# Kernel optimization log

Hardware: AMD Instinct MI355X
Metric: run time of the kernel (lower is better)

The kernel has to match this reference:

```python
import jax, jax.numpy as jnp
import numpy as np

B, S, H = 2, 512, 768
E, M, R, R2 = 64, 64, 128, 128
NER_C, REL_C, SIZE_E, CLS = 10, 8, 32, 101
NEG = -1e30


def _linear(x, w, b):
    # torch nn.Linear convention: w is [out, in]
    return x @ w.T + b


def _span_pool(emb, masks):
    # emb [B,S,H], masks [B,K,S] -> masked max over tokens -> [B,K,H]
    neg = jnp.where(masks[..., None] != 0, 0.0, NEG)  # [B,K,S,1]
    return jnp.max(neg + emb[:, None, :, :], axis=2)


def _classify_spans(input_ids, emb, masks, size_emb, rep_w, rep_b, head_w, head_b):
    pool = _span_pool(emb, masks)                      # [B,K,H]
    cls_idx = jnp.argmax((input_ids == CLS).astype(jnp.int32), axis=1)
    ctx = emb[jnp.arange(emb.shape[0]), cls_idx]       # [B,H] (get_token)
    rep = jnp.concatenate([jnp.broadcast_to(ctx[:, None, :], pool.shape), pool, size_emb], axis=-1)
    clf = _linear(jax.nn.relu(_linear(rep, rep_w, rep_b)), head_w, head_b)
    return clf, pool


def _classify_relations(pool, size_emb, rels, rel_masks, emb, w1, b1, w2, b2, w3, b3):
    Bc = pool.shape[0]
    bidx = jnp.arange(Bc)[:, None, None]
    pairs = pool[bidx, rels].reshape(Bc, rels.shape[1], -1)        # [B,R,2H]
    size_pairs = size_emb[bidx, rels].reshape(Bc, rels.shape[1], -1)  # [B,R,2*SIZE_E]
    # masked max over context tokens (rel mask)
    ctx = jnp.max(jnp.where(rel_masks[..., None] != 0, 0.0, NEG) + emb[:, None, :, :], axis=2)
    ctx = jnp.where(jnp.any(rel_masks != 0, axis=-1)[..., None], ctx, 0.0)
    rel_repr = jnp.concatenate([ctx, pairs, size_pairs], axis=-1)  # [B,R,3H+2*SIZE_E]
    h = jax.nn.relu(_linear(rel_repr, w1, b1))
    h = jax.nn.relu(_linear(h, w2, b2))
    return _linear(h, w3, b3)


def setup_inputs():
    key = jax.random.key(0)
    ks = jax.random.split(key, 24)
    p = lambda k, shape: jax.random.normal(k, shape, jnp.float32) * 0.02
    ids = jax.random.randint(ks[0], (B, S), 2000, 30000)
    ids = ids.at[:, 0].set(CLS)  # exactly one cls token per row
    return dict(
        input_ids=ids,
        entity_masks=jax.random.randint(ks[1], (B, E, S), 0, 2).astype(jnp.int32),
        entity_sizes=jax.random.randint(ks[2], (B, E), 0, 100),
        mention_masks=jax.random.randint(ks[3], (B, M, S), 0, 2).astype(jnp.int32),
        mention_sizes=jax.random.randint(ks[4], (B, M), 0, 100),
        relations=jax.random.randint(ks[5], (B, R, 2), 0, E),
        rel_masks=jax.random.randint(ks[6], (B, R, S), 0, 2).astype(jnp.int32),
        references=jax.random.randint(ks[7], (B, R2, 2), 0, M),
        references_masks=jax.random.randint(ks[8], (B, R2, S), 0, 2).astype(jnp.int32),
        token_embedding=jax.random.normal(ks[9], (B, S, H), jnp.float32),
        ner_size_emb=p(ks[10], (100, SIZE_E)),
        emd_size_emb=p(ks[11], (100, SIZE_E)),
        ner_rep_w=p(ks[12], (H, 2 * H + SIZE_E)), ner_rep_b=jnp.zeros(H, jnp.float32),
        ner_head_w=p(ks[13], (NER_C, H)), ner_head_b=jnp.zeros(NER_C, jnp.float32),
        emd_rep_w=p(ks[14], (H, 2 * H + SIZE_E)), emd_rep_b=jnp.zeros(H, jnp.float32),
        emd_head_w=p(ks[15], (2, H)), emd_head_b=jnp.zeros(2, jnp.float32),
        rel_w1=p(ks[16], (H, 3 * H + 2 * SIZE_E)), rel_b1=jnp.zeros(H, jnp.float32),
        rel_w2=p(ks[17], (H, H)), rel_b2=jnp.zeros(H, jnp.float32),
        rel_w3=p(ks[18], (REL_C, H)), rel_b3=jnp.zeros(REL_C, jnp.float32),
        cr_w1=p(ks[19], (H, 3 * H + 2 * SIZE_E)), cr_b1=jnp.zeros(H, jnp.float32),
        cr_w2=p(ks[20], (H, H)), cr_b2=jnp.zeros(H, jnp.float32),
        cr_w3=p(ks[21], (1, H)), cr_b3=jnp.zeros(1, jnp.float32),
    )


def reference(input_ids, entity_masks, entity_sizes, mention_masks, mention_sizes,
              relations, rel_masks, references, references_masks, token_embedding,
              ner_size_emb, emd_size_emb,
              ner_rep_w, ner_rep_b, ner_head_w, ner_head_b,
              emd_rep_w, emd_rep_b, emd_head_w, emd_head_b,
              rel_w1, rel_b1, rel_w2, rel_b2, rel_w3, rel_b3,
              cr_w1, cr_b1, cr_w2, cr_b2, cr_w3, cr_b3):
    sz = ner_size_emb[entity_sizes]                                    # [B,E,SIZE_E]
    entity_clf, entity_pool = _classify_spans(input_ids, token_embedding, entity_masks, sz,
                                              ner_rep_w, ner_rep_b, ner_head_w, ner_head_b)
    rel_clf = _classify_relations(entity_pool, sz, relations, rel_masks, token_embedding,
                                  rel_w1, rel_b1, rel_w2, rel_b2, rel_w3, rel_b3)
    msz = emd_size_emb[mention_sizes]
    mention_clf, mention_pool = _classify_spans(input_ids, token_embedding, mention_masks, msz,
                                                emd_rep_w, emd_rep_b, emd_head_w, emd_head_b)
    ref_clf = _classify_relations(mention_pool, msz, references, references_masks, token_embedding,
                                  cr_w1, cr_b1, cr_w2, cr_b2, cr_w3, cr_b3)
    return entity_clf, rel_clf, mention_clf, ref_clf
```

## Files before the change

kernel.cpp:

```cpp
#include <hip/hip_runtime.h>
#include <hip/hip_bf16.h>

typedef __hip_bfloat16 bf16;
typedef __attribute__((ext_vector_type(8))) short short8;
typedef __attribute__((ext_vector_type(4))) float f32x4;

#define SS 512
#define HD 768
#define NEGC (-1e30f)

#define WOFF_NER 0
#define WOFF_EMD 1204224
#define WOFF_RW1 2408448
#define WOFF_CW1 4227072
#define WOFF_RW2 6045696
#define WOFF_CW2 6635520
#define W_TOT    7225344
#define CVT_BLOCKS (W_TOT / 4 / 256)

__global__ __launch_bounds__(256) void k_pool_cvt(
    const int* __restrict__ e_masks, const int* __restrict__ m_masks,
    const int* __restrict__ r_masks, const int* __restrict__ c_masks,
    const float* __restrict__ emb, bf16* __restrict__ part, int* __restrict__ flags,
    const float* __restrict__ s0, const float* __restrict__ s1,
    const float* __restrict__ s2, const float* __restrict__ s3,
    const float* __restrict__ s4, const float* __restrict__ s5,
    bf16* __restrict__ wdst)
{
  int bx = blockIdx.x;
  int t  = threadIdx.x;

  if (bx >= 768) {
    size_t i = ((size_t)(bx - 768) * 256 + t) * 4;
    const float* s; size_t off;
    if      (i < WOFF_EMD) { s = s0; off = i; }
    else if (i < WOFF_RW1) { s = s1; off = i - WOFF_EMD; }
    else if (i < WOFF_CW1) { s = s2; off = i - WOFF_RW1; }
    else if (i < WOFF_RW2) { s = s3; off = i - WOFF_CW1; }
    else if (i < WOFF_CW2) { s = s4; off = i - WOFF_RW2; }
    else                   { s = s5; off = i - WOFF_CW2; }
    float4 v = *(const float4*)(s + off);
    wdst[i]     = __hip_bfloat16(v.x);
    wdst[i + 1] = __hip_bfloat16(v.y);
    wdst[i + 2] = __hip_bfloat16(v.z);
    wdst[i + 3] = __hip_bfloat16(v.w);
    return;
  }

  int g  = bx % 48;
  int b  = (bx / 48) & 1;
  int sp = bx / 96;
  int j0 = g * 8;

  const int* marr; int row0;
  if      (j0 < 64)  { marr = e_masks; row0 = b*64  +  j0;        }
  else if (j0 < 128) { marr = m_masks; row0 = b*64  + (j0-64);    }
  else if (j0 < 256) { marr = r_masks; row0 = b*128 + (j0-128);   }
  else               { marr = c_masks; row0 = b*128 + (j0-256);   }

  __shared__ unsigned s_pack[64];
  __shared__ unsigned s_any;
  if (t == 0) s_any = 0u;
  __syncthreads();

  int sbase = sp * 64;
  if (t < 64) {
    unsigned w = 0;
    #pragma unroll
    for (int k = 0; k < 8; k++) {
      int mm = marr[(size_t)(row0 + k) * SS + sbase + t];
      w |= (mm != 0 ? 1u : 0u) << k;
    }
    s_pack[t] = w;
    atomicOr(&s_any, w);
  }
  __syncthreads();

  float acc[8][3];
  #pragma unroll
  for (int k = 0; k < 8; k++)
    #pragma unroll
    for (int i = 0; i < 3; i++) acc[k][i] = -INFINITY;

  const float* ebase = emb + ((size_t)b * SS + sbase) * HD;
  for (int s = 0; s < 64; s++) {
    unsigned wm = s_pack[s];
    const float* ep = ebase + (size_t)s * HD + t;
    float v0 = ep[0];
    float v1 = ep[256];
    float v2 = ep[512];
    #pragma unroll
    for (int k = 0; k < 8; k++) {
      float add = ((wm >> k) & 1u) ? 0.f : NEGC;
      acc[k][0] = fmaxf(acc[k][0], v0 + add);
      acc[k][1] = fmaxf(acc[k][1], v1 + add);
      acc[k][2] = fmaxf(acc[k][2], v2 + add);
    }
  }

  #pragma unroll
  for (int k = 0; k < 8; k++) {
    int sg = b * 384 + j0 + k;
    bf16* dst = part + ((size_t)sp * 768 + sg) * HD;
    dst[t]       = __hip_bfloat16(acc[k][0]);
    dst[t + 256] = __hip_bfloat16(acc[k][1]);
    dst[t + 512] = __hip_bfloat16(acc[k][2]);
  }
  if (t < 8) flags[sp * 768 + b * 384 + j0 + t] = (int)((s_any >> t) & 1u);
}

__global__ __launch_bounds__(256) void k_combine(
    const bf16* __restrict__ part, const int* __restrict__ flags,
    bf16* __restrict__ epool, bf16* __restrict__ mpool,
    bf16* __restrict__ rctx, bf16* __restrict__ cctx)
{
  int sg = blockIdx.x;
  int b = sg / 384, j = sg % 384;
  int any = 0;
  #pragma unroll
  for (int sp = 0; sp < 8; sp++) any |= flags[sp * 768 + sg];
  #pragma unroll
  for (int i = 0; i < 3; i++) {
    int h = threadIdx.x + i * 256;
    float v = -INFINITY;
    #pragma unroll
    for (int sp = 0; sp < 8; sp++)
      v = fmaxf(v, (float)part[((size_t)sp * 768 + sg) * HD + h]);
    if      (j < 64)  epool[((size_t)b*64  + j)       * HD + h] = __hip_bfloat16(v);
    else if (j < 128) mpool[((size_t)b*64  + (j-64))  * HD + h] = __hip_bfloat16(v);
    else if (j < 256) rctx [((size_t)b*128 + (j-128)) * HD + h] = __hip_bfloat16(any ? v : 0.f);
    else              cctx [((size_t)b*128 + (j-256)) * HD + h] = __hip_bfloat16(any ? v : 0.f);
  }
}

__global__ __launch_bounds__(256) void k_rep(
    const int* __restrict__ input_ids, const float* __restrict__ emb,
    const bf16* __restrict__ epool, const bf16* __restrict__ mpool,
    const bf16* __restrict__ rctx, const bf16* __restrict__ cctx,
    const int* __restrict__ esizes, const int* __restrict__ msizes,
    const float* __restrict__ nsemb, const float* __restrict__ esemb,
    const int* __restrict__ relations, const int* __restrict__ references,
    bf16* __restrict__ nrep, bf16* __restrict__ erep,
    bf16* __restrict__ rrep, bf16* __restrict__ crep)
{
  int mode = blockIdx.y;
  if (mode < 2) {
    if (blockIdx.x >= 128) return;
    int which = mode;
    int row = blockIdx.x;
    int b = row >> 6;
    const bf16*  pool  = which ? mpool  : epool;
    const int*   sizes = which ? msizes : esizes;
    const float* st    = which ? esemb  : nsemb;
    bf16* rep = (which ? erep : nrep) + (size_t)row * 1568;

    __shared__ int s_cls;
    if (threadIdx.x == 0) s_cls = SS;
    __syncthreads();
    for (int s = threadIdx.x; s < SS; s += 256)
      if (input_ids[b * SS + s] == 101) atomicMin(&s_cls, s);
    __syncthreads();
    int ci = (s_cls == SS) ? 0 : s_cls;

    const float* ctx = emb + ((size_t)b * SS + ci) * HD;
    const bf16*  pl  = pool + (size_t)row * HD;
    for (int h = threadIdx.x; h < HD; h += 256) {
      rep[h]       = __hip_bfloat16(ctx[h]);
      rep[768 + h] = pl[h];
    }
    if (threadIdx.x < 32)
      rep[1536 + threadIdx.x] = __hip_bfloat16(st[(size_t)sizes[row] * 32 + threadIdx.x]);
  } else {
    int which = mode - 2;
    int row = blockIdx.x;
    int b = row >> 7;
    const int*   rel   = which ? references : relations;
    const bf16*  ctx   = which ? cctx   : rctx;
    const bf16*  pool  = which ? mpool  : epool;
    const int*   sizes = which ? msizes : esizes;
    const float* st    = which ? esemb  : nsemb;
    bf16* rep = (which ? crep : rrep) + (size_t)row * 2368;

    int a0 = rel[row * 2], a1 = rel[row * 2 + 1];
    const bf16* p0 = pool + ((size_t)b * 64 + a0) * HD;
    const bf16* p1 = pool + ((size_t)b * 64 + a1) * HD;
    const bf16* cx = ctx + (size_t)row * HD;
    for (int h = threadIdx.x; h < HD; h += 256) {
      rep[h]        = cx[h];
      rep[768 + h]  = p0[h];
      rep[1536 + h] = p1[h];
    }
    if (threadIdx.x < 32) {
      rep[2304 + threadIdx.x] = __hip_bfloat16(st[(size_t)sizes[b * 64 + a0] * 32 + threadIdx.x]);
      rep[2336 + threadIdx.x] = __hip_bfloat16(st[(size_t)sizes[b * 64 + a1] * 32 + threadIdx.x]);
    }
  }
}

struct GemmArgs  { const void* A; const void* W; const float* bias; void* C; int K; int M; int store_bf16; };
struct GemmArgs4 { GemmArgs p[4]; };

__global__ __launch_bounds__(256) void k_gemm4(GemmArgs4 ga)
{
  GemmArgs g = ga.p[blockIdx.z];
  int mt = blockIdx.x * 32;
  if (mt >= g.M) return;
  int nt = blockIdx.y * 32;

  const short* A = (const short*)g.A;
  const short* W = (const short*)g.W;
  int K_ = g.K;

  int wave = threadIdx.x >> 6, lane = threadIdx.x & 63;
  int lm = lane & 15, quad = lane >> 4;

  const short* a0p = A + (size_t)(mt + lm)      * K_ + quad * 8;
  const short* a1p = A + (size_t)(mt + 16 + lm) * K_ + quad * 8;
  const short* w0p = W + (size_t)(nt + lm)      * K_ + quad * 8;
  const short* w1p = W + (size_t)(nt + 16 + lm) * K_ + quad * 8;

  f32x4 acc00 = {0.f,0.f,0.f,0.f}, acc01 = {0.f,0.f,0.f,0.f};
  f32x4 acc10 = {0.f,0.f,0.f,0.f}, acc11 = {0.f,0.f,0.f,0.f};

  for (int k0 = wave * 32; k0 < K_; k0 += 128) {
    short8 a0 = *(const short8*)(a0p + k0);
    short8 a1 = *(const short8*)(a1p + k0);
    short8 w0 = *(const short8*)(w0p + k0);
    short8 w1 = *(const short8*)(w1p + k0);
    acc00 = __builtin_amdgcn_mfma_f32_16x16x32_bf16(a0, w0, acc00, 0, 0, 0);
    acc01 = __builtin_amdgcn_mfma_f32_16x16x32_bf16(a0, w1, acc01, 0, 0, 0);
    acc10 = __builtin_amdgcn_mfma_f32_16x16x32_bf16(a1, w0, acc10, 0, 0, 0);
    acc11 = __builtin_amdgcn_mfma_f32_16x16x32_bf16(a1, w1, acc11, 0, 0, 0);
  }

  __shared__ float red[4][32][32];
  #pragma unroll
  for (int reg = 0; reg < 4; reg++) {
    int r = quad * 4 + reg;
    red[wave][r][lm]           = acc00[reg];
    red[wave][r][16 + lm]      = acc01[reg];
    red[wave][16 + r][lm]      = acc10[reg];
    red[wave][16 + r][16 + lm] = acc11[reg];
  }
  __syncthreads();

  int c = threadIdx.x & 31;
  int rb = threadIdx.x >> 5;
  float bb = g.bias[nt + c];
  #pragma unroll
  for (int i = 0; i < 4; i++) {
    int r = rb + 8 * i;
    float v = red[0][r][c] + red[1][r][c] + red[2][r][c] + red[3][r][c];
    v = fmaxf(v + bb, 0.f);
    if (g.store_bf16) ((bf16*)g.C)[(size_t)(mt + r) * HD + nt + c] = __hip_bfloat16(v);
    else              ((float*)g.C)[(size_t)(mt + r) * HD + nt + c] = v;
  }
}

__global__ __launch_bounds__(256) void k_heads(
    const float* __restrict__ NH, const float* __restrict__ EH,
    const float* __restrict__ RH2, const float* __restrict__ CH2,
    const float* __restrict__ nhw, const float* __restrict__ nhb,
    const float* __restrict__ ehw, const float* __restrict__ ehb,
    const float* __restrict__ rw3, const float* __restrict__ rb3,
    const float* __restrict__ cw3, const float* __restrict__ cb3,
    float* __restrict__ out)
{
  int gr = blockIdx.x;
  const float* A; const float* W; const float* Bb; float* op; int N;
  if (gr < 128)      { A = NH  + (size_t)gr * HD;        W = nhw; Bb = nhb; N = 10; op = out + (size_t)gr * 10; }
  else if (gr < 384) { int r = gr - 128; A = RH2 + (size_t)r * HD; W = rw3; Bb = rb3; N = 8; op = out + 1280 + (size_t)r * 8; }
  else if (gr < 512) { int r = gr - 384; A = EH  + (size_t)r * HD; W = ehw; Bb = ehb; N = 2; op = out + 3328 + (size_t)r * 2; }
  else               { int r = gr - 512; A = CH2 + (size_t)r * HD; W = cw3; Bb = cb3; N = 1; op = out + 3584 + (size_t)r; }

  float acc[10];
  #pragma unroll
  for (int o = 0; o < 10; o++) acc[o] = 0.f;

  for (int k = threadIdx.x; k < HD; k += 256) {
    float a = A[k];
    #pragma unroll
    for (int o = 0; o < 10; o++) {
      int oo = (o < N) ? o : 0;
      acc[o] += a * W[(size_t)oo * HD + k];
    }
  }

  __shared__ float red[4][10];
  int lane = threadIdx.x & 63, wv = threadIdx.x >> 6;
  #pragma unroll
  for (int o = 0; o < 10; o++) {
    float v = acc[o];
    for (int off = 32; off > 0; off >>= 1) v += __shfl_down(v, off);
    if (lane == 0) red[wv][o] = v;
  }
  __syncthreads();
  if (threadIdx.x < N) {
    float v = red[0][threadIdx.x] + red[1][threadIdx.x] + red[2][threadIdx.x] +
              red[3][threadIdx.x] + Bb[threadIdx.x];
    op[threadIdx.x] = v;
  }
}

extern "C" void kernel_launch(void* const* d_in, const int* in_sizes, int n_in,
                              void* d_out, int out_size, void* d_ws, size_t ws_size,
                              hipStream_t stream)
{
  const int*   input_ids  = (const int*)d_in[0];
  const int*   e_masks    = (const int*)d_in[1];
  const int*   e_sizes    = (const int*)d_in[2];
  const int*   m_masks    = (const int*)d_in[3];
  const int*   m_sizes    = (const int*)d_in[4];
  const int*   relations  = (const int*)d_in[5];
  const int*   r_masks    = (const int*)d_in[6];
  const int*   references = (const int*)d_in[7];
  const int*   c_masks    = (const int*)d_in[8];
  const float* emb        = (const float*)d_in[9];
  const float* nsemb      = (const float*)d_in[10];
  const float* esemb      = (const float*)d_in[11];
  const float* ner_rep_w  = (const float*)d_in[12];
  const float* ner_rep_b  = (const float*)d_in[13];
  const float* ner_head_w = (const float*)d_in[14];
  const float* ner_head_b = (const float*)d_in[15];
  const float* emd_rep_w  = (const float*)d_in[16];
  const float* emd_rep_b  = (const float*)d_in[17];
  const float* emd_head_w = (const float*)d_in[18];
  const float* emd_head_b = (const float*)d_in[19];
  const float* rel_w1 = (const float*)d_in[20];
  const float* rel_b1 = (const float*)d_in[21];
  const float* rel_w2 = (const float*)d_in[22];
  const float* rel_b2 = (const float*)d_in[23];
  const float* rel_w3 = (const float*)d_in[24];
  const float* rel_b3 = (const float*)d_in[25];
  const float* cr_w1 = (const float*)d_in[26];
  const float* cr_b1 = (const float*)d_in[27];
  const float* cr_w2 = (const float*)d_in[28];
  const float* cr_b2 = (const float*)d_in[29];
  const float* cr_w3 = (const float*)d_in[30];
  const float* cr_b3 = (const float*)d_in[31];
  float* out = (float*)d_out;

  float* wsf = (float*)d_ws;
  size_t o = 0;
  int*   FLAGS = (int*)(wsf + o); o += 8 * 768;
  float* NH  = wsf + o; o += (size_t)128 * HD;
  float* EH  = wsf + o; o += (size_t)128 * HD;
  float* RH2 = wsf + o; o += (size_t)256 * HD;
  float* CH2 = wsf + o; o += (size_t)256 * HD;

  bf16* wsb = (bf16*)(wsf + o);
  size_t ob = 0;
  bf16* WBF   = wsb + ob; ob += (size_t)W_TOT;
  bf16* PART  = wsb + ob; ob += (size_t)8 * 768 * HD;
  bf16* EPOOL = wsb + ob; ob += (size_t)128 * HD;
  bf16* MPOOL = wsb + ob; ob += (size_t)128 * HD;
  bf16* RCTX  = wsb + ob; ob += (size_t)256 * HD;
  bf16* CCTX  = wsb + ob; ob += (size_t)256 * HD;
  bf16* NREP  = wsb + ob; ob += (size_t)128 * 1568;
  bf16* EREP  = wsb + ob; ob += (size_t)128 * 1568;
  bf16* RREP  = wsb + ob; ob += (size_t)256 * 2368;
  bf16* CREP  = wsb + ob; ob += (size_t)256 * 2368;
  bf16* RH1   = wsb + ob; ob += (size_t)256 * HD;
  bf16* CH1   = wsb + ob; ob += (size_t)256 * HD;

  k_pool_cvt<<<768 + CVT_BLOCKS, 256, 0, stream>>>(
      e_masks, m_masks, r_masks, c_masks, emb, PART, FLAGS,
      ner_rep_w, emd_rep_w, rel_w1, cr_w1, rel_w2, cr_w2, WBF);
  k_combine<<<768, 256, 0, stream>>>(PART, FLAGS, EPOOL, MPOOL, RCTX, CCTX);
  k_rep<<<dim3(256, 4), 256, 0, stream>>>(input_ids, emb, EPOOL, MPOOL, RCTX, CCTX,
                                          e_sizes, m_sizes, nsemb, esemb,
                                          relations, references,
                                          NREP, EREP, RREP, CREP);
  {
    GemmArgs4 ga;
    ga.p[0] = { NREP, WBF + WOFF_NER, ner_rep_b, NH,  1568, 128, 0 };
    ga.p[1] = { EREP, WBF + WOFF_EMD, emd_rep_b, EH,  1568, 128, 0 };
    ga.p[2] = { RREP, WBF + WOFF_RW1, rel_b1,    RH1, 2368, 256, 1 };
    ga.p[3] = { CREP, WBF + WOFF_CW1, cr_b1,     CH1, 2368, 256, 1 };
    k_gemm4<<<dim3(8, 24, 4), 256, 0, stream>>>(ga);
  }
  {
    GemmArgs4 ga;
    ga.p[0] = { RH1, WBF + WOFF_RW2, rel_b2, RH2, 768, 256, 0 };
    ga.p[1] = { CH1, WBF + WOFF_CW2, cr_b2,  CH2, 768, 256, 0 };
    ga.p[2] = ga.p[0]; ga.p[3] = ga.p[1];
    k_gemm4<<<dim3(8, 24, 2), 256, 0, stream>>>(ga);
  }
  k_heads<<<768, 256, 0, stream>>>(NH, EH, RH2, CH2,
                                   ner_head_w, ner_head_b, emd_head_w, emd_head_b,
                                   rel_w3, rel_b3, cr_w3, cr_b3, out);
}
```

Measured before the change: 209.2 us.

## Fuse post-pool stages into persistent megakernel with grid barriers, split pooling finer

Replaces the combine, rep-building, two GEMM and head kernels with one persistent 768-block kernel that separates stages with a software grid barrier built on global atomics. This removes several kernel launches and their gaps. The pooling kernel now splits tokens into 16 chunks of 32 instead of 8 of 64, and weight conversion is spread across the pool blocks with a strided loop. The barrier depends on all 768 blocks being co-resident (launch bounds ask for 3 blocks per CU), and the finer split doubles the partial-buffer traffic.

```diff
diff --git a/kernel.cpp b/kernel.cpp
--- a/kernel.cpp
+++ b/kernel.cpp
@@ -8,6 +8,9 @@
 #define SS 512
 #define HD 768
 #define NEGC (-1e30f)
+#define NSPLIT 16
+#define TOK 32
+#define POOL_BLOCKS 1536
 
 #define WOFF_NER 0
 #define WOFF_EMD 1204224
@@ -16,7 +19,29 @@
 #define WOFF_RW2 6045696
 #define WOFF_CW2 6635520
 #define W_TOT    7225344
-#define CVT_BLOCKS (W_TOT / 4 / 256)
+#define CVT_UNITS (W_TOT / 1024)
+
+__device__ unsigned d_cnt = 0;
+__device__ unsigned d_gen = 0;
+
+__device__ __forceinline__ void grid_bar(int nblk)
+{
+  __syncthreads();
+  if (threadIdx.x == 0) {
+    __threadfence();
+    unsigned g = atomicAdd(&d_gen, 0u);
+    unsigned t = atomicAdd(&d_cnt, 1u);
+    if (t == (unsigned)(nblk - 1)) {
+      atomicExch(&d_cnt, 0u);
+      __threadfence();
+      atomicAdd(&d_gen, 1u);
+    } else {
+      while (atomicAdd(&d_gen, 0u) == g) { __builtin_amdgcn_s_sleep(2); }
+    }
+    __threadfence();
+  }
+  __syncthreads();
+}
 
 __global__ __launch_bounds__(256) void k_pool_cvt(
     const int* __restrict__ e_masks, const int* __restrict__ m_masks,
@@ -30,8 +55,8 @@
   int bx = blockIdx.x;
   int t  = threadIdx.x;
 
-  if (bx >= 768) {
-    size_t i = ((size_t)(bx - 768) * 256 + t) * 4;
+  for (int u = bx; u < CVT_UNITS; u += POOL_BLOCKS) {
+    size_t i = ((size_t)u * 256 + t) * 4;
     const float* s; size_t off;
     if      (i < WOFF_EMD) { s = s0; off = i; }
     else if (i < WOFF_RW1) { s = s1; off = i - WOFF_EMD; }
@@ -44,7 +69,6 @@
     wdst[i + 1] = __hip_bfloat16(v.y);
     wdst[i + 2] = __hip_bfloat16(v.z);
     wdst[i + 3] = __hip_bfloat16(v.w);
-    return;
   }
 
   int g  = bx % 48;
@@ -58,13 +82,13 @@
   else if (j0 < 256) { marr = r_masks; row0 = b*128 + (j0-128);   }
   else               { marr = c_masks; row0 = b*128 + (j0-256);   }
 
-  __shared__ unsigned s_pack[64];
+  __shared__ unsigned s_pack[TOK];
   __shared__ unsigned s_any;
   if (t == 0) s_any = 0u;
   __syncthreads();
 
-  int sbase = sp * 64;
-  if (t < 64) {
+  int sbase = sp * TOK;
+  if (t < TOK) {
     unsigned w = 0;
     #pragma unroll
     for (int k = 0; k < 8; k++) {
@@ -83,7 +107,7 @@
     for (int i = 0; i < 3; i++) acc[k][i] = -INFINITY;
 
   const float* ebase = emb + ((size_t)b * SS + sbase) * HD;
-  for (int s = 0; s < 64; s++) {
+  for (int s = 0; s < TOK; s++) {
     unsigned wm = s_pack[s];
     const float* ep = ebase + (size_t)s * HD + t;
     float v0 = ep[0];
@@ -109,104 +133,28 @@
   if (t < 8) flags[sp * 768 + b * 384 + j0 + t] = (int)((s_any >> t) & 1u);
 }
 
-__global__ __launch_bounds__(256) void k_combine(
-    const bf16* __restrict__ part, const int* __restrict__ flags,
-    bf16* __restrict__ epool, bf16* __restrict__ mpool,
-    bf16* __restrict__ rctx, bf16* __restrict__ cctx)
+struct GemmArgs { const void* A; const void* W; const float* bias; void* C; int K; int M; int store_bf16; };
+
+struct MegaArgs {
+  const bf16* part; const int* flags;
+  bf16 *epool, *mpool, *rctx, *cctx;
+  const int* input_ids; const float* emb;
+  const int *esizes, *msizes;
+  const float *nsemb, *esemb;
+  const int *relations, *references;
+  bf16 *nrep, *erep, *rrep, *crep;
+  GemmArgs g1[4];
+  GemmArgs g2[2];
+  const float *NH, *EH, *RH2, *CH2;
+  const float *nhw, *nhb, *ehw, *ehb, *rw3, *rb3, *cw3, *cb3;
+  float* out;
+};
+
+__device__ __forceinline__ void gemm_stage(const GemmArgs& g, int x, int y, float* smem)
 {
-  int sg = blockIdx.x;
-  int b = sg / 384, j = sg % 384;
-  int any = 0;
-  #pragma unroll
-  for (int sp = 0; sp < 8; sp++) any |= flags[sp * 768 + sg];
-  #pragma unroll
-  for (int i = 0; i < 3; i++) {
-    int h = threadIdx.x + i * 256;
-    float v = -INFINITY;
-    #pragma unroll
-    for (int sp = 0; sp < 8; sp++)
-      v = fmaxf(v, (float)part[((size_t)sp * 768 + sg) * HD + h]);
-    if      (j < 64)  epool[((size_t)b*64  + j)       * HD + h] = __hip_bfloat16(v);
-    else if (j < 128) mpool[((size_t)b*64  + (j-64))  * HD + h] = __hip_bfloat16(v);
-    else if (j < 256) rctx [((size_t)b*128 + (j-128)) * HD + h] = __hip_bfloat16(any ? v : 0.f);
-    else              cctx [((size_t)b*128 + (j-256)) * HD + h] = __hip_bfloat16(any ? v : 0.f);
-  }
-}
-
-__global__ __launch_bounds__(256) void k_rep(
-    const int* __restrict__ input_ids, const float* __restrict__ emb,
-    const bf16* __restrict__ epool, const bf16* __restrict__ mpool,
-    const bf16* __restrict__ rctx, const bf16* __restrict__ cctx,
-    const int* __restrict__ esizes, const int* __restrict__ msizes,
-    const float* __restrict__ nsemb, const float* __restrict__ esemb,
-    const int* __restrict__ relations, const int* __restrict__ references,
-    bf16* __restrict__ nrep, bf16* __restrict__ erep,
-    bf16* __restrict__ rrep, bf16* __restrict__ crep)
-{
-  int mode = blockIdx.y;
-  if (mode < 2) {
-    if (blockIdx.x >= 128) return;
-    int which = mode;
-    int row = blockIdx.x;
-    int b = row >> 6;
-    const bf16*  pool  = which ? mpool  : epool;
-    const int*   sizes = which ? msizes : esizes;
-    const float* st    = which ? esemb  : nsemb;
-    bf16* rep = (which ? erep : nrep) + (size_t)row * 1568;
-
-    __shared__ int s_cls;
-    if (threadIdx.x == 0) s_cls = SS;
-    __syncthreads();
-    for (int s = threadIdx.x; s < SS; s += 256)
-      if (input_ids[b * SS + s] == 101) atomicMin(&s_cls, s);
-    __syncthreads();
-    int ci = (s_cls == SS) ? 0 : s_cls;
-
-    const float* ctx = emb + ((size_t)b * SS + ci) * HD;
-    const bf16*  pl  = pool + (size_t)row * HD;
-    for (int h = threadIdx.x; h < HD; h += 256) {
-      rep[h]       = __hip_bfloat16(ctx[h]);
-      rep[768 + h] = pl[h];
-    }
-    if (threadIdx.x < 32)
-      rep[1536 + threadIdx.x] = __hip_bfloat16(st[(size_t)sizes[row] * 32 + threadIdx.x]);
-  } else {
-    int which = mode - 2;
-    int row = blockIdx.x;
-    int b = row >> 7;
-    const int*   rel   = which ? references : relations;
-    const bf16*  ctx   = which ? cctx   : rctx;
-    const bf16*  pool  = which ? mpool  : epool;
-    const int*   sizes = which ? msizes : esizes;
-    const float* st    = which ? esemb  : nsemb;
-    bf16* rep = (which ? crep : rrep) + (size_t)row * 2368;
-
-    int a0 = rel[row * 2], a1 = rel[row * 2 + 1];
-    const bf16* p0 = pool + ((size_t)b * 64 + a0) * HD;
-    const bf16* p1 = pool + ((size_t)b * 64 + a1) * HD;
-    const bf16* cx = ctx + (size_t)row * HD;
-    for (int h = threadIdx.x; h < HD; h += 256) {
-      rep[h]        = cx[h];
-      rep[768 + h]  = p0[h];
-      rep[1536 + h] = p1[h];
-    }
-    if (threadIdx.x < 32) {
-      rep[2304 + threadIdx.x] = __hip_bfloat16(st[(size_t)sizes[b * 64 + a0] * 32 + threadIdx.x]);
-      rep[2336 + threadIdx.x] = __hip_bfloat16(st[(size_t)sizes[b * 64 + a1] * 32 + threadIdx.x]);
-    }
-  }
-}
-
-struct GemmArgs  { const void* A; const void* W; const float* bias; void* C; int K; int M; int store_bf16; };
-struct GemmArgs4 { GemmArgs p[4]; };
-
-__global__ __launch_bounds__(256) void k_gemm4(GemmArgs4 ga)
-{
-  GemmArgs g = ga.p[blockIdx.z];
-  int mt = blockIdx.x * 32;
+  int mt = x * 32;
   if (mt >= g.M) return;
-  int nt = blockIdx.y * 32;
-
+  int nt = y * 32;
   const short* A = (const short*)g.A;
   const short* W = (const short*)g.W;
   int K_ = g.K;
@@ -233,14 +181,13 @@
     acc11 = __builtin_amdgcn_mfma_f32_16x16x32_bf16(a1, w1, acc11, 0, 0, 0);
   }
 
-  __shared__ float red[4][32][32];
   #pragma unroll
   for (int reg = 0; reg < 4; reg++) {
     int r = quad * 4 + reg;
-    red[wave][r][lm]           = acc00[reg];
-    red[wave][r][16 + lm]      = acc01[reg];
-    red[wave][16 + r][lm]      = acc10[reg];
-    red[wave][16 + r][16 + lm] = acc11[reg];
+    smem[wave*1024 + r*32 + lm]             = acc00[reg];
+    smem[wave*1024 + r*32 + 16 + lm]        = acc01[reg];
+    smem[wave*1024 + (16 + r)*32 + lm]      = acc10[reg];
+    smem[wave*1024 + (16 + r)*32 + 16 + lm] = acc11[reg];
   }
   __syncthreads();
 
@@ -250,55 +197,147 @@
   #pragma unroll
   for (int i = 0; i < 4; i++) {
     int r = rb + 8 * i;
-    float v = red[0][r][c] + red[1][r][c] + red[2][r][c] + red[3][r][c];
+    float v = smem[r*32 + c] + smem[1024 + r*32 + c] + smem[2048 + r*32 + c] + smem[3072 + r*32 + c];
     v = fmaxf(v + bb, 0.f);
     if (g.store_bf16) ((bf16*)g.C)[(size_t)(mt + r) * HD + nt + c] = __hip_bfloat16(v);
     else              ((float*)g.C)[(size_t)(mt + r) * HD + nt + c] = v;
   }
+  __syncthreads();
 }
 
-__global__ __launch_bounds__(256) void k_heads(
-    const float* __restrict__ NH, const float* __restrict__ EH,
-    const float* __restrict__ RH2, const float* __restrict__ CH2,
-    const float* __restrict__ nhw, const float* __restrict__ nhb,
-    const float* __restrict__ ehw, const float* __restrict__ ehb,
-    const float* __restrict__ rw3, const float* __restrict__ rb3,
-    const float* __restrict__ cw3, const float* __restrict__ cb3,
-    float* __restrict__ out)
+#define MEGA_BLOCKS 768
+
+__global__ __launch_bounds__(256, 3) void k_mega(MegaArgs a)
 {
-  int gr = blockIdx.x;
-  const float* A; const float* W; const float* Bb; float* op; int N;
-  if (gr < 128)      { A = NH  + (size_t)gr * HD;        W = nhw; Bb = nhb; N = 10; op = out + (size_t)gr * 10; }
-  else if (gr < 384) { int r = gr - 128; A = RH2 + (size_t)r * HD; W = rw3; Bb = rb3; N = 8; op = out + 1280 + (size_t)r * 8; }
-  else if (gr < 512) { int r = gr - 384; A = EH  + (size_t)r * HD; W = ehw; Bb = ehb; N = 2; op = out + 3328 + (size_t)r * 2; }
-  else               { int r = gr - 512; A = CH2 + (size_t)r * HD; W = cw3; Bb = cb3; N = 1; op = out + 3584 + (size_t)r; }
-
-  float acc[10];
-  #pragma unroll
-  for (int o = 0; o < 10; o++) acc[o] = 0.f;
-
-  for (int k = threadIdx.x; k < HD; k += 256) {
-    float a = A[k];
+  __shared__ float smem[4 * 32 * 32];
+  __shared__ int s_cls;
+  int t = threadIdx.x;
+
+  {
+    int sg = blockIdx.x;
+    int b = sg / 384, j = sg % 384;
+    int any = 0;
+    #pragma unroll
+    for (int sp = 0; sp < NSPLIT; sp++) any |= a.flags[sp * 768 + sg];
+    #pragma unroll
+    for (int i = 0; i < 3; i++) {
+      int h = t + i * 256;
+      float v = -INFINITY;
+      #pragma unroll
+      for (int sp = 0; sp < NSPLIT; sp++)
+        v = fmaxf(v, (float)a.part[((size_t)sp * 768 + sg) * HD + h]);
+      if      (j < 64)  a.epool[((size_t)b*64  + j)       * HD + h] = __hip_bfloat16(v);
+      else if (j < 128) a.mpool[((size_t)b*64  + (j-64))  * HD + h] = __hip_bfloat16(v);
+      else if (j < 256) a.rctx [((size_t)b*128 + (j-128)) * HD + h] = __hip_bfloat16(any ? v : 0.f);
+      else              a.cctx [((size_t)b*128 + (j-256)) * HD + h] = __hip_bfloat16(any ? v : 0.f);
+    }
+  }
+  grid_bar(MEGA_BLOCKS);
+
+  for (int u = blockIdx.x; u < 1024; u += MEGA_BLOCKS) {
+    int mode = u >> 8, x = u & 255;
+    if (mode < 2) {
+      if (x >= 128) continue;
+      int which = mode;
+      int row = x;
+      int b = row >> 6;
+      const bf16*  pool  = which ? a.mpool  : a.epool;
+      const int*   sizes = which ? a.msizes : a.esizes;
+      const float* st    = which ? a.esemb  : a.nsemb;
+      bf16* rep = (which ? a.erep : a.nrep) + (size_t)row * 1568;
+
+      if (t == 0) s_cls = SS;
+      __syncthreads();
+      for (int s = t; s < SS; s += 256)
+        if (a.input_ids[b * SS + s] == 101) atomicMin(&s_cls, s);
+      __syncthreads();
+      int ci = (s_cls == SS) ? 0 : s_cls;
+
+      const float* ctx = a.emb + ((size_t)b * SS + ci) * HD;
+      const bf16*  pl  = pool + (size_t)row * HD;
+      for (int h = t; h < HD; h += 256) {
+        rep[h]       = __hip_bfloat16(ctx[h]);
+        rep[768 + h] = pl[h];
+      }
+      if (t < 32)
+        rep[1536 + t] = __hip_bfloat16(st[(size_t)sizes[row] * 32 + t]);
+      __syncthreads();
+    } else {
+      int which = mode - 2;
+      int row = x;
+      int b = row >> 7;
+      const int*   rel   = which ? a.references : a.relations;
+      const bf16*  ctx   = which ? a.cctx   : a.rctx;
+      const bf16*  pool  = which ? a.mpool  : a.epool;
+      const int*   sizes = which ? a.msizes : a.esizes;
+      const float* st    = which ? a.esemb  : a.nsemb;
+      bf16* rep = (which ? a.crep : a.rrep) + (size_t)row * 2368;
+
+      int a0 = rel[row * 2], a1 = rel[row * 2 + 1];
+      const bf16* p0 = pool + ((size_t)b * 64 + a0) * HD;
+      const bf16* p1 = pool + ((size_t)b * 64 + a1) * HD;
+      const bf16* cx = ctx + (size_t)row * HD;
+      for (int h = t; h < HD; h += 256) {
+        rep[h]        = cx[h];
+        rep[768 + h]  = p0[h];
+        rep[1536 + h] = p1[h];
+      }
+      if (t < 32) {
+        rep[2304 + t] = __hip_bfloat16(st[(size_t)sizes[b * 64 + a0] * 32 + t]);
+        rep[2336 + t] = __hip_bfloat16(st[(size_t)sizes[b * 64 + a1] * 32 + t]);
+      }
+    }
+  }
+  grid_bar(MEGA_BLOCKS);
+
+  {
+    int u = blockIdx.x;
+    int x = u & 7, y = (u >> 3) % 24, z = u / 192;
+    gemm_stage(a.g1[z], x, y, smem);
+  }
+  grid_bar(MEGA_BLOCKS);
+
+  if (blockIdx.x < 384) {
+    int u = blockIdx.x;
+    int x = u & 7, y = (u >> 3) % 24, z = u / 192;
+    gemm_stage(a.g2[z], x, y, smem);
+  }
+  grid_bar(MEGA_BLOCKS);
+
+  {
+    int gr = blockIdx.x;
+    const float* A; const float* W; const float* Bb; float* op; int N;
+    if (gr < 128)      { A = a.NH  + (size_t)gr * HD;        W = a.nhw; Bb = a.nhb; N = 10; op = a.out + (size_t)gr * 10; }
+    else if (gr < 384) { int r = gr - 128; A = a.RH2 + (size_t)r * HD; W = a.rw3; Bb = a.rb3; N = 8; op = a.out + 1280 + (size_t)r * 8; }
+    else if (gr < 512) { int r = gr - 384; A = a.EH  + (size_t)r * HD; W = a.ehw; Bb = a.ehb; N = 2; op = a.out + 3328 + (size_t)r * 2; }
+    else               { int r = gr - 512; A = a.CH2 + (size_t)r * HD; W = a.cw3; Bb = a.cb3; N = 1; op = a.out + 3584 + (size_t)r; }
+
+    float acc[10];
+    #pragma unroll
+    for (int o = 0; o < 10; o++) acc[o] = 0.f;
+
+    for (int k = t; k < HD; k += 256) {
+      float av = A[k];
+      #pragma unroll
+      for (int o = 0; o < 10; o++) {
+        int oo = (o < N) ? o : 0;
+        acc[o] += av * W[(size_t)oo * HD + k];
+      }
+    }
+
+    float* red = smem;
+    int lane = t & 63, wv = t >> 6;
     #pragma unroll
     for (int o = 0; o < 10; o++) {
-      int oo = (o < N) ? o : 0;
-      acc[o] += a * W[(size_t)oo * HD + k];
-    }
-  }
-
-  __shared__ float red[4][10];
-  int lane = threadIdx.x & 63, wv = threadIdx.x >> 6;
-  #pragma unroll
-  for (int o = 0; o < 10; o++) {
-    float v = acc[o];
-    for (int off = 32; off > 0; off >>= 1) v += __shfl_down(v, off);
-    if (lane == 0) red[wv][o] = v;
-  }
-  __syncthreads();
-  if (threadIdx.x < N) {
-    float v = red[0][threadIdx.x] + red[1][threadIdx.x] + red[2][threadIdx.x] +
-              red[3][threadIdx.x] + Bb[threadIdx.x];
-    op[threadIdx.x] = v;
+      float v = acc[o];
+      for (int off = 32; off > 0; off >>= 1) v += __shfl_down(v, off);
+      if (lane == 0) red[wv * 10 + o] = v;
+    }
+    __syncthreads();
+    if (t < N) {
+      float v = red[0 * 10 + t] + red[1 * 10 + t] + red[2 * 10 + t] + red[3 * 10 + t] + Bb[t];
+      op[t] = v;
+    }
   }
 }
 
@@ -342,7 +381,7 @@
 
   float* wsf = (float*)d_ws;
   size_t o = 0;
-  int*   FLAGS = (int*)(wsf + o); o += 8 * 768;
+  int*   FLAGS = (int*)(wsf + o); o += NSPLIT * 768;
   float* NH  = wsf + o; o += (size_t)128 * HD;
   float* EH  = wsf + o; o += (size_t)128 * HD;
   float* RH2 = wsf + o; o += (size_t)256 * HD;
@@ -351,7 +390,7 @@
   bf16* wsb = (bf16*)(wsf + o);
   size_t ob = 0;
   bf16* WBF   = wsb + ob; ob += (size_t)W_TOT;
-  bf16* PART  = wsb + ob; ob += (size_t)8 * 768 * HD;
+  bf16* PART  = wsb + ob; ob += (size_t)NSPLIT * 768 * HD;
   bf16* EPOOL = wsb + ob; ob += (size_t)128 * HD;
   bf16* MPOOL = wsb + ob; ob += (size_t)128 * HD;
   bf16* RCTX  = wsb + ob; ob += (size_t)256 * HD;
@@ -363,30 +402,30 @@
   bf16* RH1   = wsb + ob; ob += (size_t)256 * HD;
   bf16* CH1   = wsb + ob; ob += (size_t)256 * HD;
 
-  k_pool_cvt<<<768 + CVT_BLOCKS, 256, 0, stream>>>(
+  k_pool_cvt<<<POOL_BLOCKS, 256, 0, stream>>>(
       e_masks, m_masks, r_masks, c_masks, emb, PART, FLAGS,
       ner_rep_w, emd_rep_w, rel_w1, cr_w1, rel_w2, cr_w2, WBF);
-  k_combine<<<768, 256, 0, stream>>>(PART, FLAGS, EPOOL, MPOOL, RCTX, CCTX);
-  k_rep<<<dim3(256, 4), 256, 0, stream>>>(input_ids, emb, EPOOL, MPOOL, RCTX, CCTX,
-                                          e_sizes, m_sizes, nsemb, esemb,
-                                          relations, references,
-                                          NREP, EREP, RREP, CREP);
-  {
-    GemmArgs4 ga;
-    ga.p[0] = { NREP, WBF + WOFF_NER, ner_rep_b, NH,  1568, 128, 0 };
-    ga.p[1] = { EREP, WBF + WOFF_EMD, emd_rep_b, EH,  1568, 128, 0 };
-    ga.p[2] = { RREP, WBF + WOFF_RW1, rel_b1,    RH1, 2368, 256, 1 };
-    ga.p[3] = { CREP, WBF + WOFF_CW1, cr_b1,     CH1, 2368, 256, 1 };
-    k_gemm4<<<dim3(8, 24, 4), 256, 0, stream>>>(ga);
-  }
-  {
-    GemmArgs4 ga;
-    ga.p[0] = { RH1, WBF + WOFF_RW2, rel_b2, RH2, 768, 256, 0 };
-    ga.p[1] = { CH1, WBF + WOFF_CW2, cr_b2,  CH2, 768, 256, 0 };
-    ga.p[2] = ga.p[0]; ga.p[3] = ga.p[1];
-    k_gemm4<<<dim3(8, 24, 2), 256, 0, stream>>>(ga);
-  }
-  k_heads<<<768, 256, 0, stream>>>(NH, EH, RH2, CH2,
-                                   ner_head_w, ner_head_b, emd_head_w, emd_head_b,
-                                   rel_w3, rel_b3, cr_w3, cr_b3, out);
+
+  MegaArgs ma;
+  ma.part = PART; ma.flags = FLAGS;
+  ma.epool = EPOOL; ma.mpool = MPOOL; ma.rctx = RCTX; ma.cctx = CCTX;
+  ma.input_ids = input_ids; ma.emb = emb;
+  ma.esizes = e_sizes; ma.msizes = m_sizes;
+  ma.nsemb = nsemb; ma.esemb = esemb;
+  ma.relations = relations; ma.references = references;
+  ma.nrep = NREP; ma.erep = EREP; ma.rrep = RREP; ma.crep = CREP;
+  ma.g1[0] = { NREP, WBF + WOFF_NER, ner_rep_b, NH,  1568, 128, 0 };
+  ma.g1[1] = { EREP, WBF + WOFF_EMD, emd_rep_b, EH,  1568, 128, 0 };
+  ma.g1[2] = { RREP, WBF + WOFF_RW1, rel_b1,    RH1, 2368, 256, 1 };
+  ma.g1[3] = { CREP, WBF + WOFF_CW1, cr_b1,     CH1, 2368, 256, 1 };
+  ma.g2[0] = { RH1, WBF + WOFF_RW2, rel_b2, RH2, 768, 256, 0 };
+  ma.g2[1] = { CH1, WBF + WOFF_CW2, cr_b2,  CH2, 768, 256, 0 };
+  ma.NH = NH; ma.EH = EH; ma.RH2 = RH2; ma.CH2 = CH2;
+  ma.nhw = ner_head_w; ma.nhb = ner_head_b;
+  ma.ehw = emd_head_w; ma.ehb = emd_head_b;
+  ma.rw3 = rel_w3; ma.rb3 = rel_b3;
+  ma.cw3 = cr_w3;  ma.cb3 = cr_b3;
+  ma.out = out;
+
+  k_mega<<<MEGA_BLOCKS, 256, 0, stream>>>(ma);
 }
```

Result: slower. 525.7 us (+151.4%).
